# Performance work log

Measured on AMD Instinct MI355X. Metric: run time of the kernel, lower is better.

The kernel has to match this reference:

```python
import jax, jax.numpy as jnp
import numpy as np

N, C_IN, H, W = 48, 64, 128, 128


def _conv3x3(x, w, b):
    # NCHW conv, kernel 3, stride 1, pad 1 (SAME)
    y = jax.lax.conv_general_dilated(
        x, w, window_strides=(1, 1), padding=((1, 1), (1, 1)),
        dimension_numbers=("NCHW", "OIHW", "NCHW"))
    return y + b[None, :, None, None]


def setup_inputs() -> dict:
    key = jax.random.key(0)
    ks = jax.random.split(key, 4)
    s1 = 1.0 / np.sqrt(C_IN * 9)
    s2 = 1.0 / np.sqrt(128 * 9)
    s3 = 1.0 / np.sqrt(32 * 9)
    return {
        "x": jax.random.normal(ks[0], (N, C_IN, H, W), dtype=jnp.float32),
        "to_process": jnp.arange(N, dtype=jnp.int64) if jax.config.jax_enable_x64 else jnp.arange(N, dtype=jnp.int32),
        "batch_size": 8,
        "W1": jax.random.normal(ks[1], (128, C_IN, 3, 3), dtype=jnp.float32) * s1,
        "b1": jnp.zeros((128,), dtype=jnp.float32),
        "W2": jax.random.normal(ks[2], (32, 128, 3, 3), dtype=jnp.float32) * s2,
        "b2": jnp.zeros((32,), dtype=jnp.float32),
        "W3": jax.random.normal(ks[3], (1, 32, 3, 3), dtype=jnp.float32) * s3,
        "b3": jnp.zeros((1,), dtype=jnp.float32),
    }


def reference(x, to_process, batch_size, W1, b1, W2, b2, W3, b3):
    # x holds only the active sites listed in to_process; all ops are per-site.
    x = jax.nn.relu(_conv3x3(x, W1, b1))          # [N,128,H,W]
    x = jax.nn.relu(_conv3x3(x, W2, b2))          # [N,32,H,W]
    n, c, h, w = x.shape
    # SparseBilinearUpsample(2): half-pixel-center bilinear x2 (align_corners=False)
    x = jax.image.resize(x, (n, c, 2 * h, 2 * w), method="bilinear")
    x = _conv3x3(x, W3, b3)                        # [N,1,2H,2W]
    return x
```

## Files before the change

### kernel.cpp

```cpp
#include <hip/hip_runtime.h>


typedef _Float16 half_t;
typedef _Float16 half2_t __attribute__((ext_vector_type(2)));
typedef _Float16 half4_t __attribute__((ext_vector_type(4)));
typedef _Float16 half8   __attribute__((ext_vector_type(8)));
typedef float    floatx4  __attribute__((ext_vector_type(4)));
typedef float    floatx16 __attribute__((ext_vector_type(16)));

__global__ __launch_bounds__(256) void repack_w(
    const float* __restrict__ W1, const float* __restrict__ W2,
    const float* __restrict__ W3, half_t* __restrict__ wh1,
    half_t* __restrict__ wh2, half_t* __restrict__ wh3)
{
    int idx = blockIdx.x * 256 + threadIdx.x;
    if (idx < 73728) {
        int ci = idx & 63, co = (idx >> 6) & 127, tap = idx >> 13;
        wh1[idx] = (half_t)W1[(co * 64 + ci) * 9 + tap];
    } else if (idx < 110592) {
        int j = idx - 73728;
        int ci = j & 127, co = (j >> 7) & 31, tap = j >> 12;
        wh2[j] = (half_t)W2[(co * 128 + ci) * 9 + tap];
    } else if (idx < 110880) {
        int j = idx - 110592;
        int ci = j & 31, tap = j >> 5;
        wh3[j] = (half_t)W3[ci * 9 + tap];
    }
}

__global__ __launch_bounds__(256) void repack_x(
    const float* __restrict__ x, half_t* __restrict__ xh)
{
    const int tid = threadIdx.x;
    const int px = tid & 127, rr = tid >> 7;
    const int y = blockIdx.x * 2 + rr;
    const int n = blockIdx.y;
    const float* xn = x + (size_t)n * 64 * 16384 + (size_t)y * 128 + px;
    half2_t hb[32];
#pragma unroll
    for (int c2 = 0; c2 < 32; ++c2) {
        float f0 = xn[(size_t)(2 * c2) * 16384];
        float f1 = xn[(size_t)(2 * c2 + 1) * 16384];
        half2_t h; h.x = (half_t)f0; h.y = (half_t)f1;
        hb[c2] = h;
    }
    half_t* op = xh + (((size_t)n * 128 + y) * 128 + px) * 64;
#pragma unroll
    for (int k = 0; k < 8; ++k)
        *(half8*)(op + k * 8) = *(half8*)(&hb[k * 4]);
}

__global__ __launch_bounds__(256, 2) void conv1_mfma(
    const half_t* __restrict__ xh,
    const half_t* __restrict__ wh,
    const float*  __restrict__ bias,
    half_t* __restrict__ y1h)
{
    __shared__ half_t lx[10 * 34 * 72];
    const int tid  = threadIdx.x;
    const int lane = tid & 63;
    const int wave = tid >> 6;
    const int l31 = lane & 31, lq = lane >> 5;
    const int wco = wave >> 1, wpx = wave & 1;
    const int x0 = blockIdx.x * 32, y0 = blockIdx.y * 8;
    const int n = blockIdx.z;
    const half_t* xn = xh + (size_t)n * (128 * 128 * 64);

    for (int idx = tid; idx < 10 * 34 * 8; idx += 256) {
        int ch = idx & 7;
        int col = (idx >> 3) % 34;
        int row = (idx >> 3) / 34;
        int gx = x0 - 1 + col, gy = y0 - 1 + row;
        half8 v = {};
        if ((unsigned)gx < 128u && (unsigned)gy < 128u)
            v = *(const half8*)(xn + ((size_t)gy * 128 + gx) * 64 + ch * 8);
        *(half8*)(&lx[(row * 34 + col) * 72 + ch * 8]) = v;
    }
    __syncthreads();

    floatx16 acc[2][4] = {};

#pragma unroll
    for (int tap = 0; tap < 9; ++tap) {
        const int dy = tap / 3, dx = tap % 3;
        const half_t* wt = wh + tap * (128 * 64) + (wco * 64 + l31) * 64 + lq * 8;
        const half_t* bp = &lx[((wpx * 4 + dy) * 34 + l31 + dx) * 72 + lq * 8];
#pragma unroll
        for (int kc = 0; kc < 4; ++kc) {
            half8 a0 = *(const half8*)(wt + kc * 16);
            half8 a1 = *(const half8*)(wt + 32 * 64 + kc * 16);
            half8 b[4];
#pragma unroll
            for (int nf = 0; nf < 4; ++nf)
                b[nf] = *(const half8*)(bp + nf * (34 * 72) + kc * 16);
#pragma unroll
            for (int nf = 0; nf < 4; ++nf) {
                acc[0][nf] = __builtin_amdgcn_mfma_f32_32x32x16_f16(a0, b[nf], acc[0][nf], 0, 0, 0);
                acc[1][nf] = __builtin_amdgcn_mfma_f32_32x32x16_f16(a1, b[nf], acc[1][nf], 0, 0, 0);
            }
        }
    }

#pragma unroll
    for (int mf = 0; mf < 2; ++mf) {
        int co0 = wco * 64 + mf * 32 + lq * 4;
#pragma unroll
        for (int nf = 0; nf < 4; ++nf) {
            floatx16 A = acc[mf][nf];
            int oy = y0 + wpx * 4 + nf, ox = x0 + l31;
            half_t* op = y1h + (((size_t)n * 128 + oy) * 128 + ox) * 128 + co0;
#pragma unroll
            for (int g = 0; g < 4; ++g) {
                floatx4 bv = *(const floatx4*)(bias + co0 + 8 * g);
                half4_t o;
                o.x = (half_t)fmaxf(A[4 * g + 0] + bv.x, 0.f);
                o.y = (half_t)fmaxf(A[4 * g + 1] + bv.y, 0.f);
                o.z = (half_t)fmaxf(A[4 * g + 2] + bv.z, 0.f);
                o.w = (half_t)fmaxf(A[4 * g + 3] + bv.w, 0.f);
                *(half4_t*)(op + 8 * g) = o;
            }
        }
    }
}

__global__ __launch_bounds__(256, 3) void conv2_mfma(
    const half_t* __restrict__ y1h,
    const half_t* __restrict__ wh,
    const float*  __restrict__ bias,
    half_t* __restrict__ y2h)
{
    __shared__ half_t lx[18 * 34 * 40];
    const int tid  = threadIdx.x;
    const int lane = tid & 63;
    const int w    = tid >> 6;
    const int l15 = lane & 15, quad = lane >> 4;
    const int x0 = blockIdx.x * 32, y0 = blockIdx.y * 16;
    const int n = blockIdx.z;
    const half_t* yn = y1h + (size_t)n * (128 * 128 * 128);

    floatx4 acc[2][8] = {};

    for (int h = 0; h < 4; ++h) {
        for (int idx = tid; idx < 18 * 34 * 4; idx += 256) {
            int ch = idx & 3;
            int col = (idx >> 2) % 34;
            int row = (idx >> 2) / 34;
            int gx = x0 - 1 + col, gy = y0 - 1 + row;
            half8 v = {};
            if ((unsigned)gx < 128u && (unsigned)gy < 128u)
                v = *(const half8*)(yn + ((size_t)gy * 128 + gx) * 128 + h * 32 + ch * 8);
            *(half8*)(&lx[(row * 34 + col) * 40 + ch * 8]) = v;
        }
        __syncthreads();
#pragma unroll
        for (int tap = 0; tap < 9; ++tap) {
            const int dy = tap / 3, dx = tap % 3;
            const half_t* wt = wh + tap * (32 * 128) + l15 * 128 + h * 32 + quad * 8;
            half8 a0 = *(const half8*)(wt);
            half8 a1 = *(const half8*)(wt + 16 * 128);
#pragma unroll
            for (int nf = 0; nf < 8; ++nf) {
                int rr = w * 4 + (nf >> 1) + dy;
                int cc = (nf & 1) * 16 + l15 + dx;
                half8 b = *(const half8*)(&lx[(rr * 34 + cc) * 40 + quad * 8]);
                acc[0][nf] = __builtin_amdgcn_mfma_f32_16x16x32_f16(a0, b, acc[0][nf], 0, 0, 0);
                acc[1][nf] = __builtin_amdgcn_mfma_f32_16x16x32_f16(a1, b, acc[1][nf], 0, 0, 0);
            }
        }
        __syncthreads();
    }

#pragma unroll
    for (int mf = 0; mf < 2; ++mf) {
        int co0 = mf * 16 + quad * 4;
        floatx4 bv = *(const floatx4*)(bias + co0);
#pragma unroll
        for (int nf = 0; nf < 8; ++nf) {
            int oy = y0 + w * 4 + (nf >> 1), ox = x0 + (nf & 1) * 16 + l15;
            floatx4 A = acc[mf][nf];
            half4_t o;
            o.x = (half_t)fmaxf(A.x + bv.x, 0.f);
            o.y = (half_t)fmaxf(A.y + bv.y, 0.f);
            o.z = (half_t)fmaxf(A.z + bv.z, 0.f);
            o.w = (half_t)fmaxf(A.w + bv.w, 0.f);
            *(half4_t*)(y2h + (((size_t)n * 128 + oy) * 128 + ox) * 32 + co0) = o;
        }
    }
}

__global__ __launch_bounds__(256) void upsample_k(
    const half_t* __restrict__ y2h, half_t* __restrict__ uh)
{
    int idx = blockIdx.x * 256 + threadIdx.x;
    int X = idx & 255, Y = (idx >> 8) & 255, n = idx >> 16;
    int jx = X >> 1, jy = Y >> 1;
    int jxo = (X & 1) ? (jx < 127 ? jx + 1 : 127) : (jx > 0 ? jx - 1 : 0);
    int jyo = (Y & 1) ? (jy < 127 ? jy + 1 : 127) : (jy > 0 ? jy - 1 : 0);
    const half_t* base = y2h + (size_t)n * (128 * 128 * 32);
    const half_t* p00 = base + ((size_t)jy  * 128 + jx ) * 32;
    const half_t* p01 = base + ((size_t)jy  * 128 + jxo) * 32;
    const half_t* p10 = base + ((size_t)jyo * 128 + jx ) * 32;
    const half_t* p11 = base + ((size_t)jyo * 128 + jxo) * 32;
    half_t* op = uh + (((size_t)n * 256 + Y) * 256 + X) * 32;
#pragma unroll
    for (int c = 0; c < 4; ++c) {
        half8 v00 = *(const half8*)(p00 + c * 8);
        half8 v01 = *(const half8*)(p01 + c * 8);
        half8 v10 = *(const half8*)(p10 + c * 8);
        half8 v11 = *(const half8*)(p11 + c * 8);
        half8 o = v00 * (half_t)0.5625f + (v01 + v10) * (half_t)0.1875f
                + v11 * (half_t)0.0625f;
        *(half8*)(op + c * 8) = o;
    }
}

__global__ __launch_bounds__(256) void conv3_k(
    const half_t* __restrict__ uh,
    const half_t* __restrict__ wh3,
    const float*  __restrict__ bias,
    float* __restrict__ out)
{
    __shared__ half_t lu[10 * 34 * 40];
    const int tid = threadIdx.x;
    const int c = tid & 31, r = tid >> 5;
    const int x0 = blockIdx.x * 32, y0 = blockIdx.y * 8;
    const int n = blockIdx.z;
    const half_t* un = uh + (size_t)n * (256 * 256 * 32);

    for (int idx = tid; idx < 10 * 34 * 4; idx += 256) {
        int ch = idx & 3;
        int col = (idx >> 2) % 34;
        int row = (idx >> 2) / 34;
        int gx = x0 - 1 + col, gy = y0 - 1 + row;
        half8 v = {};
        if ((unsigned)gx < 256u && (unsigned)gy < 256u)
            v = *(const half8*)(un + ((size_t)gy * 256 + gx) * 32 + ch * 8);
        *(half8*)(&lu[(row * 34 + col) * 40 + ch * 8]) = v;
    }
    __syncthreads();

    float acc = 0.f;
#pragma unroll
    for (int tap = 0; tap < 9; ++tap) {
        const int dy = tap / 3, dx = tap % 3;
        const half_t* lp = &lu[((r + dy) * 34 + c + dx) * 40];
        const half_t* wp = wh3 + tap * 32;
#pragma unroll
        for (int cc = 0; cc < 4; ++cc) {
            half8 v = *(const half8*)(lp + cc * 8);
            half8 w = *(const half8*)(wp + cc * 8);
            acc = __builtin_amdgcn_fdot2(__builtin_shufflevector(v, v, 0, 1),
                                         __builtin_shufflevector(w, w, 0, 1), acc, false);
            acc = __builtin_amdgcn_fdot2(__builtin_shufflevector(v, v, 2, 3),
                                         __builtin_shufflevector(w, w, 2, 3), acc, false);
            acc = __builtin_amdgcn_fdot2(__builtin_shufflevector(v, v, 4, 5),
                                         __builtin_shufflevector(w, w, 4, 5), acc, false);
            acc = __builtin_amdgcn_fdot2(__builtin_shufflevector(v, v, 6, 7),
                                         __builtin_shufflevector(w, w, 6, 7), acc, false);
        }
    }
    out[((size_t)n * 256 + (y0 + r)) * 256 + x0 + c] = acc + bias[0];
}

extern "C" void kernel_launch(void* const* d_in, const int* in_sizes, int n_in,
                              void* d_out, int out_size, void* d_ws, size_t ws_size,
                              hipStream_t stream) {
    const float* x  = (const float*)d_in[0];
    const float* W1 = (const float*)d_in[3];
    const float* b1 = (const float*)d_in[4];
    const float* W2 = (const float*)d_in[5];
    const float* b2 = (const float*)d_in[6];
    const float* W3 = (const float*)d_in[7];
    const float* b3 = (const float*)d_in[8];
    float* out = (float*)d_out;

    char* ws = (char*)d_ws;
    half_t* xh  = (half_t*)ws;
    half_t* uh  = (half_t*)ws;
    half_t* y1h = (half_t*)(ws + 201326592ull);
    half_t* y2h = (half_t*)(ws + 402653184ull);
    half_t* wh1 = (half_t*)(ws + 452984832ull);
    half_t* wh2 = wh1 + 73728;
    half_t* wh3 = wh2 + 36864;

    repack_w<<<434, 256, 0, stream>>>(W1, W2, W3, wh1, wh2, wh3);
    repack_x<<<dim3(64, 48), 256, 0, stream>>>(x, xh);
    conv1_mfma<<<dim3(4, 16, 48), 256, 0, stream>>>(xh, wh1, b1, y1h);
    conv2_mfma<<<dim3(4, 8, 48), 256, 0, stream>>>(y1h, wh2, b2, y2h);
    upsample_k<<<12288, 256, 0, stream>>>(y2h, uh);
    conv3_k<<<dim3(8, 32, 48), 256, 0, stream>>>(uh, wh3, b3, out);
}
```

Baseline: 834.2 us.

## Fuse bilinear upsample into conv3 tile load and prefetch conv1 weights per tap

The separate upsample kernel is removed. conv3 now computes the bilinear x2 interpolation directly from y2 while filling its shared-memory tile, so the 4x-sized upsampled intermediate is never written to or read back from global memory. Separately, conv1 double-buffers its per-tap weight fragments in registers, issuing the global loads for the next tap before the MFMAs of the current one. The trade-offs are some redundant interpolation loads at tile halos and higher register pressure in conv1.

```diff
diff --git a/kernel.cpp b/kernel.cpp
--- a/kernel.cpp
+++ b/kernel.cpp
@@ -76,6 +76,16 @@
             v = *(const half8*)(xn + ((size_t)gy * 128 + gx) * 64 + ch * 8);
         *(half8*)(&lx[(row * 34 + col) * 72 + ch * 8]) = v;
     }
+
+    const half_t* wbase = wh + (wco * 64 + l31) * 64 + lq * 8;
+
+    half8 w[2][8];
+#pragma unroll
+    for (int k = 0; k < 4; ++k) {
+        w[0][2 * k]     = *(const half8*)(wbase + k * 16);
+        w[0][2 * k + 1] = *(const half8*)(wbase + 32 * 64 + k * 16);
+    }
+
     __syncthreads();
 
     floatx16 acc[2][4] = {};
@@ -83,20 +93,26 @@
 #pragma unroll
     for (int tap = 0; tap < 9; ++tap) {
         const int dy = tap / 3, dx = tap % 3;
-        const half_t* wt = wh + tap * (128 * 64) + (wco * 64 + l31) * 64 + lq * 8;
+        const int cur = tap & 1, nxt = cur ^ 1;
+        if (tap < 8) {
+            const half_t* wn = wbase + (tap + 1) * (128 * 64);
+#pragma unroll
+            for (int k = 0; k < 4; ++k) {
+                w[nxt][2 * k]     = *(const half8*)(wn + k * 16);
+                w[nxt][2 * k + 1] = *(const half8*)(wn + 32 * 64 + k * 16);
+            }
+        }
         const half_t* bp = &lx[((wpx * 4 + dy) * 34 + l31 + dx) * 72 + lq * 8];
 #pragma unroll
         for (int kc = 0; kc < 4; ++kc) {
-            half8 a0 = *(const half8*)(wt + kc * 16);
-            half8 a1 = *(const half8*)(wt + 32 * 64 + kc * 16);
             half8 b[4];
 #pragma unroll
             for (int nf = 0; nf < 4; ++nf)
                 b[nf] = *(const half8*)(bp + nf * (34 * 72) + kc * 16);
 #pragma unroll
             for (int nf = 0; nf < 4; ++nf) {
-                acc[0][nf] = __builtin_amdgcn_mfma_f32_32x32x16_f16(a0, b[nf], acc[0][nf], 0, 0, 0);
-                acc[1][nf] = __builtin_amdgcn_mfma_f32_32x32x16_f16(a1, b[nf], acc[1][nf], 0, 0, 0);
+                acc[0][nf] = __builtin_amdgcn_mfma_f32_32x32x16_f16(w[cur][2 * kc],     b[nf], acc[0][nf], 0, 0, 0);
+                acc[1][nf] = __builtin_amdgcn_mfma_f32_32x32x16_f16(w[cur][2 * kc + 1], b[nf], acc[1][nf], 0, 0, 0);
             }
         }
     }
@@ -188,34 +204,8 @@
     }
 }
 
-__global__ __launch_bounds__(256) void upsample_k(
-    const half_t* __restrict__ y2h, half_t* __restrict__ uh)
-{
-    int idx = blockIdx.x * 256 + threadIdx.x;
-    int X = idx & 255, Y = (idx >> 8) & 255, n = idx >> 16;
-    int jx = X >> 1, jy = Y >> 1;
-    int jxo = (X & 1) ? (jx < 127 ? jx + 1 : 127) : (jx > 0 ? jx - 1 : 0);
-    int jyo = (Y & 1) ? (jy < 127 ? jy + 1 : 127) : (jy > 0 ? jy - 1 : 0);
-    const half_t* base = y2h + (size_t)n * (128 * 128 * 32);
-    const half_t* p00 = base + ((size_t)jy  * 128 + jx ) * 32;
-    const half_t* p01 = base + ((size_t)jy  * 128 + jxo) * 32;
-    const half_t* p10 = base + ((size_t)jyo * 128 + jx ) * 32;
-    const half_t* p11 = base + ((size_t)jyo * 128 + jxo) * 32;
-    half_t* op = uh + (((size_t)n * 256 + Y) * 256 + X) * 32;
-#pragma unroll
-    for (int c = 0; c < 4; ++c) {
-        half8 v00 = *(const half8*)(p00 + c * 8);
-        half8 v01 = *(const half8*)(p01 + c * 8);
-        half8 v10 = *(const half8*)(p10 + c * 8);
-        half8 v11 = *(const half8*)(p11 + c * 8);
-        half8 o = v00 * (half_t)0.5625f + (v01 + v10) * (half_t)0.1875f
-                + v11 * (half_t)0.0625f;
-        *(half8*)(op + c * 8) = o;
-    }
-}
-
-__global__ __launch_bounds__(256) void conv3_k(
-    const half_t* __restrict__ uh,
+__global__ __launch_bounds__(256) void conv3_fused(
+    const half_t* __restrict__ y2h,
     const half_t* __restrict__ wh3,
     const float*  __restrict__ bias,
     float* __restrict__ out)
@@ -225,17 +215,30 @@
     const int c = tid & 31, r = tid >> 5;
     const int x0 = blockIdx.x * 32, y0 = blockIdx.y * 8;
     const int n = blockIdx.z;
-    const half_t* un = uh + (size_t)n * (256 * 256 * 32);
+    const half_t* base = y2h + (size_t)n * (128 * 128 * 32);
 
     for (int idx = tid; idx < 10 * 34 * 4; idx += 256) {
-        int ch = idx & 3;
-        int col = (idx >> 2) % 34;
-        int row = (idx >> 2) / 34;
-        int gx = x0 - 1 + col, gy = y0 - 1 + row;
-        half8 v = {};
-        if ((unsigned)gx < 256u && (unsigned)gy < 256u)
-            v = *(const half8*)(un + ((size_t)gy * 256 + gx) * 32 + ch * 8);
-        *(half8*)(&lu[(row * 34 + col) * 40 + ch * 8]) = v;
+        int cc = idx & 3;
+        int p  = idx >> 2;
+        int col = p % 34, row = p / 34;
+        int X = x0 - 1 + col, Y = y0 - 1 + row;
+        half8 o = {};
+        if ((unsigned)X < 256u && (unsigned)Y < 256u) {
+            int jx = X >> 1, jy = Y >> 1;
+            int jxo = (X & 1) ? (jx < 127 ? jx + 1 : 127) : (jx > 0 ? jx - 1 : 0);
+            int jyo = (Y & 1) ? (jy < 127 ? jy + 1 : 127) : (jy > 0 ? jy - 1 : 0);
+            const half_t* p00 = base + ((size_t)jy  * 128 + jx ) * 32 + cc * 8;
+            const half_t* p01 = base + ((size_t)jy  * 128 + jxo) * 32 + cc * 8;
+            const half_t* p10 = base + ((size_t)jyo * 128 + jx ) * 32 + cc * 8;
+            const half_t* p11 = base + ((size_t)jyo * 128 + jxo) * 32 + cc * 8;
+            half8 v00 = *(const half8*)p00;
+            half8 v01 = *(const half8*)p01;
+            half8 v10 = *(const half8*)p10;
+            half8 v11 = *(const half8*)p11;
+            o = v00 * (half_t)0.5625f + (v01 + v10) * (half_t)0.1875f
+              + v11 * (half_t)0.0625f;
+        }
+        *(half8*)(&lu[(row * 34 + col) * 40 + cc * 8]) = o;
     }
     __syncthreads();
 
@@ -276,7 +279,6 @@
 
     char* ws = (char*)d_ws;
     half_t* xh  = (half_t*)ws;
-    half_t* uh  = (half_t*)ws;
     half_t* y1h = (half_t*)(ws + 201326592ull);
     half_t* y2h = (half_t*)(ws + 402653184ull);
     half_t* wh1 = (half_t*)(ws + 452984832ull);
@@ -287,6 +289,5 @@
     repack_x<<<dim3(64, 48), 256, 0, stream>>>(x, xh);
     conv1_mfma<<<dim3(4, 16, 48), 256, 0, stream>>>(xh, wh1, b1, y1h);
     conv2_mfma<<<dim3(4, 8, 48), 256, 0, stream>>>(y1h, wh2, b2, y2h);
-    upsample_k<<<12288, 256, 0, stream>>>(y2h, uh);
-    conv3_k<<<dim3(8, 32, 48), 256, 0, stream>>>(uh, wh3, b3, out);
-}
+    conv3_fused<<<dim3(8, 32, 48), 256, 0, stream>>>(y2h, wh3, b3, out);
+}
```

Result: faster. 746.1 us (-10.6%).
